# Performance work log

Measured on AMD Instinct MI355X. Metric: run time of the kernel, lower is better.

## Reference

```python
import jax, jax.numpy as jnp
import numpy as np

N_HEAD = 12

def setup_inputs() -> dict:
    key = jax.random.key(0)
    ks = jax.random.split(key, 5)
    B, T, C = 8, 1024, 768
    s = 0.02
    return {
        'x': jax.random.normal(ks[0], (B, T, C), dtype=jnp.float32),
        'w_attn': jax.random.normal(ks[1], (C, 3 * C), dtype=jnp.float32) * s,
        'b_attn': jax.random.normal(ks[2], (3 * C,), dtype=jnp.float32) * s,
        'w_proj': jax.random.normal(ks[3], (C, C), dtype=jnp.float32) * s,
        'b_proj': jax.random.normal(ks[4], (C,), dtype=jnp.float32) * s,
    }

def reference(x, w_attn, b_attn, w_proj, b_proj):
    B, T, C = x.shape
    H, D = N_HEAD, C // N_HEAD
    qkv = x @ w_attn + b_attn                      # [B,T,3C]
    q, k, v = jnp.split(qkv, 3, axis=-1)
    q = q.reshape(B, T, H, D)
    k = k.reshape(B, T, H, D)
    v = v.reshape(B, T, H, D)
    # NOTE: faithful to source - NO 1/sqrt(D) scaling
    wei = jnp.einsum('bthd,bshd->bhts', q, k)      # [B,H,T,T]
    causal = jnp.tril(jnp.ones((T, T), dtype=bool))
    wei = jnp.where(causal[None, None], wei, -jnp.inf)
    wei = jax.nn.softmax(wei, axis=-1)
    out = jnp.einsum('bhts,bshd->bthd', wei, v)    # [B,T,H,D]
    out = out.reshape(B, T, C)
    return out @ w_proj + b_proj
```

## Files before the change

kernel.cpp:

```cpp
#include <hip/hip_runtime.h>

typedef __attribute__((ext_vector_type(8))) short bf16x8_t;
typedef __attribute__((ext_vector_type(4))) float f32x4_t;

#define AS1C(p) ((const __attribute__((address_space(1))) void*)(p))
#define AS3(p)  ((__attribute__((address_space(3))) void*)(p))

#define N_HEAD 12
#define SEQ_T 1024
#define CDIM 768
#define HDIM 64
#define L2E 1.44269504f

__device__ __forceinline__ unsigned short f2bf(float f) {
    union { float f; unsigned int u; } v;
    v.f = f;
    unsigned int r = (v.u + 0x7fffu + ((v.u >> 16) & 1u)) >> 16;
    return (unsigned short)r;
}

__global__ __launch_bounds__(256) void cvt_x(
    const float4* __restrict__ src, ushort4* __restrict__ dst, int n4)
{
    int i = blockIdx.x * 256 + threadIdx.x;
    if (i < n4) {
        float4 v = src[i];
        ushort4 o;
        o.x = f2bf(v.x); o.y = f2bf(v.y); o.z = f2bf(v.z); o.w = f2bf(v.w);
        dst[i] = o;
    }
}

__global__ __launch_bounds__(256) void cvt_transpose(
    const float* __restrict__ src, unsigned short* __restrict__ dst, int R, int Cc)
{
    __shared__ float tile[32][33];
    int c0 = blockIdx.x * 32, r0 = blockIdx.y * 32;
#pragma unroll
    for (int i = 0; i < 4; i++)
        tile[threadIdx.y + i * 8][threadIdx.x] =
            src[(size_t)(r0 + threadIdx.y + i * 8) * Cc + c0 + threadIdx.x];
    __syncthreads();
#pragma unroll
    for (int i = 0; i < 4; i++)
        dst[(size_t)(c0 + threadIdx.y + i * 8) * R + r0 + threadIdx.x] =
            f2bf(tile[threadIdx.x][threadIdx.y + i * 8]);
}

__device__ __forceinline__ void gemm128_core(
    const unsigned short* __restrict__ A, const unsigned short* __restrict__ Bt,
    unsigned short* As, unsigned short* Bs, f32x4_t acc[4][4], int mBase, int nBase)
{
    const int tid  = threadIdx.x;
    const int lane = tid & 63;
    const int wv   = tid >> 6;
    const int quad = lane >> 4;
    const int l16  = lane & 15;
    const int wm   = (wv >> 1) * 64;
    const int wn   = (wv & 1) * 64;

    f32x4_t zero = {0.f, 0.f, 0.f, 0.f};
#pragma unroll
    for (int tm = 0; tm < 4; tm++)
#pragma unroll
        for (int tn = 0; tn < 4; tn++)
            acc[tm][tn] = zero;

    for (int kt = 0; kt < 768; kt += 64) {
#pragma unroll
        for (int i = 0; i < 4; i++) {
            int cbase = i * 256 + wv * 64;
            int ci = cbase + lane;
            int r = ci >> 3;
            int koff = (ci & 7) << 3;
            __builtin_amdgcn_global_load_lds(
                AS1C(A + (size_t)(mBase + r) * 768 + kt + koff),
                AS3(As + cbase * 8), 16, 0, 0);
            __builtin_amdgcn_global_load_lds(
                AS1C(Bt + (size_t)(nBase + r) * 768 + kt + koff),
                AS3(Bs + cbase * 8), 16, 0, 0);
        }
        __syncthreads();
#pragma unroll
        for (int ks = 0; ks < 2; ks++) {
            bf16x8_t af[4], bfv[4];
#pragma unroll
            for (int tm = 0; tm < 4; tm++)
                af[tm] = *(const bf16x8_t*)(As + (wm + tm * 16 + l16) * 64 + ks * 32 + quad * 8);
#pragma unroll
            for (int tn = 0; tn < 4; tn++)
                bfv[tn] = *(const bf16x8_t*)(Bs + (wn + tn * 16 + l16) * 64 + ks * 32 + quad * 8);
#pragma unroll
            for (int tm = 0; tm < 4; tm++)
#pragma unroll
                for (int tn = 0; tn < 4; tn++)
                    acc[tm][tn] = __builtin_amdgcn_mfma_f32_16x16x32_bf16(
                        af[tm], bfv[tn], acc[tm][tn], 0, 0, 0);
        }
        __syncthreads();
    }
}

__global__ __launch_bounds__(256) void gemm_qkv(
    const unsigned short* __restrict__ x, const unsigned short* __restrict__ waT,
    const float* __restrict__ b_attn,
    unsigned short* __restrict__ qbuf, unsigned short* __restrict__ kbuf,
    unsigned short* __restrict__ vbuf)
{
    __shared__ __align__(16) unsigned short As[128 * 64];
    __shared__ __align__(16) unsigned short Bs[128 * 64];
    f32x4_t acc[4][4];
    const int mBase = blockIdx.y * 128;
    const int nBase = blockIdx.x * 128;
    gemm128_core(x, waT, As, Bs, acc, mBase, nBase);

    const int tid = threadIdx.x;
    const int lane = tid & 63, wv = tid >> 6;
    const int quad = lane >> 4, l16 = lane & 15;
    const int wm = (wv >> 1) * 64, wn = (wv & 1) * 64;
    const int part = blockIdx.x / 6;

#pragma unroll
    for (int tn = 0; tn < 4; tn++) {
        int n = nBase + wn + tn * 16 + l16;
        float bv = b_attn[n];
        int f = n - part * 768;
        int hh = f >> 6, d = f & 63;
        if (part == 2) {
#pragma unroll
            for (int tm = 0; tm < 4; tm++) {
                int t0 = mBase + wm + tm * 16 + quad * 4;
                int bb = t0 >> 10, tt = t0 & 1023;
                ushort4 pk;
                pk.x = f2bf(acc[tm][tn][0] + bv);
                pk.y = f2bf(acc[tm][tn][1] + bv);
                pk.z = f2bf(acc[tm][tn][2] + bv);
                pk.w = f2bf(acc[tm][tn][3] + bv);
                *(ushort4*)(vbuf + ((size_t)(bb * N_HEAD + hh) * HDIM + d) * SEQ_T + tt) = pk;
            }
        } else {
            const float scale = (part == 0) ? L2E : 1.f;
            unsigned short* dst = (part == 0) ? qbuf : kbuf;
#pragma unroll
            for (int tm = 0; tm < 4; tm++) {
#pragma unroll
                for (int i = 0; i < 4; i++) {
                    int row = mBase + wm + tm * 16 + quad * 4 + i;
                    int bb = row >> 10, tt = row & 1023;
                    dst[((size_t)(bb * N_HEAD + hh) * SEQ_T + tt) * HDIM + d] =
                        f2bf((acc[tm][tn][i] + bv) * scale);
                }
            }
        }
    }
}

__device__ __forceinline__ void attn_tile(
    const bf16x8_t qf[2], const bf16x8_t kf[4][2], const bf16x8_t vf[4][2],
    f32x4_t o[4], float lsum[4], unsigned short* pw,
    int diag, int wv, int quad, int l16)
{
    f32x4_t zero = {0.f, 0.f, 0.f, 0.f};
    f32x4_t s[4];
#pragma unroll
    for (int c = 0; c < 4; c++) {
        s[c] = zero;
#pragma unroll
        for (int kc = 0; kc < 2; kc++)
            s[c] = __builtin_amdgcn_mfma_f32_16x16x32_bf16(qf[kc], kf[c][kc], s[c], 0, 0, 0);
    }
    if (diag) {
#pragma unroll
        for (int c = 0; c < 4; c++)
#pragma unroll
            for (int i = 0; i < 4; i++)
                if (c * 16 + l16 > wv * 16 + quad * 4 + i) s[c][i] = -1e30f;
    }
    float p[4][4];
#pragma unroll
    for (int c = 0; c < 4; c++)
#pragma unroll
        for (int i = 0; i < 4; i++)
            p[c][i] = exp2f(s[c][i]);
#pragma unroll
    for (int i = 0; i < 4; i++)
        lsum[i] += (p[0][i] + p[1][i]) + (p[2][i] + p[3][i]);

    __asm__ __volatile__("" ::: "memory");
#pragma unroll
    for (int c = 0; c < 4; c++)
#pragma unroll
        for (int i = 0; i < 4; i++) {
            int m = quad * 4 + i;
            pw[m * 64 + (((2 * c + (l16 >> 3)) ^ (m & 7)) << 3) + (l16 & 7)] = f2bf(p[c][i]);
        }
    __asm__ __volatile__("" ::: "memory");
#pragma unroll
    for (int kc = 0; kc < 2; kc++) {
        bf16x8_t pf = *(const bf16x8_t*)(pw + l16 * 64 + (((kc * 4 + quad) ^ (l16 & 7)) << 3));
#pragma unroll
        for (int c = 0; c < 4; c++)
            o[c] = __builtin_amdgcn_mfma_f32_16x16x32_bf16(pf, vf[c][kc], o[c], 0, 0, 0);
    }
}

__global__ __launch_bounds__(256, 3) void attn_fused(
    const unsigned short* __restrict__ qb, const unsigned short* __restrict__ kb,
    const unsigned short* __restrict__ vb, unsigned short* __restrict__ attb)
{
    __shared__ __align__(16) unsigned short Kbuf[2][64 * 64];
    __shared__ __align__(16) unsigned short Vbuf[2][64 * 64];
    __shared__ __align__(16) unsigned short Psh[4][16 * 64];

    const int t = blockIdx.x;
    const int h = blockIdx.y;
    const int b = blockIdx.z;
    const int tid = threadIdx.x;
    const int lane = tid & 63, wv = tid >> 6;
    const int quad = lane >> 4, l16 = lane & 15;
    const int tB = 15 - t, kmax = 15 - t;

    const size_t bh = (size_t)(b * N_HEAD + h);
    const unsigned short* kbase = kb + bh * SEQ_T * HDIM;
    const unsigned short* vbase = vb + bh * HDIM * SEQ_T;
    const unsigned short* qpt   = qb + bh * SEQ_T * HDIM;

    const int j0 = wv * 128 + lane, j1 = j0 + 64;
    const int r0 = j0 >> 3, g0 = (j0 & 7) ^ (r0 & 7);
    const int r1 = j1 >> 3, g1 = (j1 & 7) ^ (r1 & 7);
    const int rgK0 = r0 * 64 + g0 * 8,   rgK1 = r1 * 64 + g1 * 8;
    const int rgV0 = r0 * 1024 + g0 * 8, rgV1 = r1 * 1024 + g1 * 8;
    const int ldsc0 = (wv * 128) * 8, ldsc1 = (wv * 128 + 64) * 8;

    bf16x8_t qfA[2], qfB[2];
    {
        const unsigned short* qa = qpt + (size_t)(t * 64 + wv * 16 + l16) * HDIM;
        const unsigned short* qbp = qpt + (size_t)(tB * 64 + wv * 16 + l16) * HDIM;
#pragma unroll
        for (int kc = 0; kc < 2; kc++) {
            qfA[kc] = *(const bf16x8_t*)(qa + kc * 32 + quad * 8);
            qfB[kc] = *(const bf16x8_t*)(qbp + kc * 32 + quad * 8);
        }
    }

    f32x4_t zero = {0.f, 0.f, 0.f, 0.f};
    f32x4_t oA[4], oB[4];
    float lA[4], lB[4];
#pragma unroll
    for (int c = 0; c < 4; c++) { oA[c] = zero; oB[c] = zero; }
#pragma unroll
    for (int i = 0; i < 4; i++) { lA[i] = 0.f; lB[i] = 0.f; }

    __builtin_amdgcn_global_load_lds(AS1C(kbase + rgK0), AS3(&Kbuf[0][0] + ldsc0), 16, 0, 0);
    __builtin_amdgcn_global_load_lds(AS1C(kbase + rgK1), AS3(&Kbuf[0][0] + ldsc1), 16, 0, 0);
    __builtin_amdgcn_global_load_lds(AS1C(vbase + rgV0), AS3(&Vbuf[0][0] + ldsc0), 16, 0, 0);
    __builtin_amdgcn_global_load_lds(AS1C(vbase + rgV1), AS3(&Vbuf[0][0] + ldsc1), 16, 0, 0);
    __syncthreads();

    for (int kt = 0; kt <= kmax; kt++) {
        const int cur = kt & 1, nxt = cur ^ 1;
        if (kt < kmax) {
            const unsigned short* kp = kbase + (kt + 1) * 4096;
            const unsigned short* vp = vbase + (kt + 1) * 64;
            __builtin_amdgcn_global_load_lds(AS1C(kp + rgK0), AS3(&Kbuf[nxt][0] + ldsc0), 16, 0, 0);
            __builtin_amdgcn_global_load_lds(AS1C(kp + rgK1), AS3(&Kbuf[nxt][0] + ldsc1), 16, 0, 0);
            __builtin_amdgcn_global_load_lds(AS1C(vp + rgV0), AS3(&Vbuf[nxt][0] + ldsc0), 16, 0, 0);
            __builtin_amdgcn_global_load_lds(AS1C(vp + rgV1), AS3(&Vbuf[nxt][0] + ldsc1), 16, 0, 0);
        }

        bf16x8_t kf[4][2], vf[4][2];
        const unsigned short* Kc = &Kbuf[cur][0];
        const unsigned short* Vc = &Vbuf[cur][0];
#pragma unroll
        for (int c = 0; c < 4; c++)
#pragma unroll
            for (int kc = 0; kc < 2; kc++) {
                int roff = (c * 16 + l16) * 64 + (((kc * 4 + quad) ^ (l16 & 7)) << 3);
                kf[c][kc] = *(const bf16x8_t*)(Kc + roff);
                vf[c][kc] = *(const bf16x8_t*)(Vc + roff);
            }

        unsigned short* pw = &Psh[wv][0];
        attn_tile(qfB, kf, vf, oB, lB, pw, kt == tB, wv, quad, l16);
        if (kt <= t)
            attn_tile(qfA, kf, vf, oA, lA, pw, kt == t, wv, quad, l16);
        __syncthreads();
    }

#pragma unroll
    for (int off = 1; off < 16; off <<= 1)
#pragma unroll
        for (int i = 0; i < 4; i++) {
            lA[i] += __shfl_xor(lA[i], off);
            lB[i] += __shfl_xor(lB[i], off);
        }
    float iA[4], iB[4];
#pragma unroll
    for (int i = 0; i < 4; i++) { iA[i] = 1.f / lA[i]; iB[i] = 1.f / lB[i]; }

#pragma unroll
    for (int c = 0; c < 4; c++)
#pragma unroll
        for (int i = 0; i < 4; i++) {
            int rowA = t * 64 + wv * 16 + quad * 4 + i;
            int rowB = tB * 64 + wv * 16 + quad * 4 + i;
            int col = h * HDIM + c * 16 + l16;
            attb[((size_t)b * SEQ_T + rowA) * CDIM + col] = f2bf(oA[c][i] * iA[i]);
            attb[((size_t)b * SEQ_T + rowB) * CDIM + col] = f2bf(oB[c][i] * iB[i]);
        }
}

__global__ __launch_bounds__(256) void gemm_proj(
    const unsigned short* __restrict__ attb, const unsigned short* __restrict__ wpT,
    const float* __restrict__ b_proj, float* __restrict__ out)
{
    __shared__ __align__(16) unsigned short As[128 * 64];
    __shared__ __align__(16) unsigned short Bs[128 * 64];
    f32x4_t acc[4][4];
    const int mBase = blockIdx.y * 128;
    const int nBase = blockIdx.x * 128;
    gemm128_core(attb, wpT, As, Bs, acc, mBase, nBase);

    const int tid = threadIdx.x;
    const int lane = tid & 63, wv = tid >> 6;
    const int quad = lane >> 4, l16 = lane & 15;
    const int wm = (wv >> 1) * 64, wn = (wv & 1) * 64;

#pragma unroll
    for (int tn = 0; tn < 4; tn++) {
        int n = nBase + wn + tn * 16 + l16;
        float bv = b_proj[n];
#pragma unroll
        for (int tm = 0; tm < 4; tm++)
#pragma unroll
            for (int i = 0; i < 4; i++) {
                int row = mBase + wm + tm * 16 + quad * 4 + i;
                out[(size_t)row * CDIM + n] = acc[tm][tn][i] + bv;
            }
    }
}

extern "C" void kernel_launch(void* const* d_in, const int* in_sizes, int n_in,
                              void* d_out, int out_size, void* d_ws, size_t ws_size,
                              hipStream_t stream) {
    const float* x      = (const float*)d_in[0];
    const float* w_attn = (const float*)d_in[1];
    const float* b_attn = (const float*)d_in[2];
    const float* w_proj = (const float*)d_in[3];
    const float* b_proj = (const float*)d_in[4];
    float* out = (float*)d_out;

    unsigned short* ws   = (unsigned short*)d_ws;
    unsigned short* waT  = ws;
    unsigned short* wpT  = waT + 1769472;
    unsigned short* xbf  = wpT + 589824;
    unsigned short* qbuf = xbf + 6291456;
    unsigned short* kbuf = qbuf + 6291456;
    unsigned short* vbuf = kbuf + 6291456;
    unsigned short* attb = vbuf + 6291456;

    cvt_x<<<dim3(6144), 256, 0, stream>>>((const float4*)x, (ushort4*)xbf, 1572864);
    cvt_transpose<<<dim3(72, 24), dim3(32, 8), 0, stream>>>(w_attn, waT, 768, 2304);
    cvt_transpose<<<dim3(24, 24), dim3(32, 8), 0, stream>>>(w_proj, wpT, 768, 768);
    gemm_qkv<<<dim3(18, 64), 256, 0, stream>>>(xbf, waT, b_attn, qbuf, kbuf, vbuf);
    attn_fused<<<dim3(8, N_HEAD, 8), 256, 0, stream>>>(qbuf, kbuf, vbuf, attb);
    gemm_proj<<<dim3(6, 64), 256, 0, stream>>>(attb, wpT, b_proj, out);
}
```

Baseline: 212.1 us.

## Swizzle GEMM LDS tiles and transpose attention score MFMA for packed P writes

The shared GEMM core now XOR-swizzles the 16-byte chunk index on both the global-to-LDS load and the fragment read, to cut LDS bank conflicts. The attention kernel computes S^T (K as the A operand, Q as B), so each lane holds one query row. The row sum therefore needs only two cross-lane shuffles, and P can be written to LDS as packed 32-bit pairs instead of scalar 16-bit stores. K fragments are now loaded per column block and shared between the two query tiles, with the extra cost of per-row inverse shuffles in the epilogue.

```diff
diff --git a/kernel.cpp b/kernel.cpp
--- a/kernel.cpp
+++ b/kernel.cpp
@@ -72,7 +72,7 @@
             int cbase = i * 256 + wv * 64;
             int ci = cbase + lane;
             int r = ci >> 3;
-            int koff = (ci & 7) << 3;
+            int koff = (((ci & 7) ^ (r & 7)) << 3);
             __builtin_amdgcn_global_load_lds(
                 AS1C(A + (size_t)(mBase + r) * 768 + kt + koff),
                 AS3(As + cbase * 8), 16, 0, 0);
@@ -86,10 +86,12 @@
             bf16x8_t af[4], bfv[4];
 #pragma unroll
             for (int tm = 0; tm < 4; tm++)
-                af[tm] = *(const bf16x8_t*)(As + (wm + tm * 16 + l16) * 64 + ks * 32 + quad * 8);
+                af[tm] = *(const bf16x8_t*)(As + (wm + tm * 16 + l16) * 64 +
+                                            (((ks * 4 + quad) ^ (l16 & 7)) << 3));
 #pragma unroll
             for (int tn = 0; tn < 4; tn++)
-                bfv[tn] = *(const bf16x8_t*)(Bs + (wn + tn * 16 + l16) * 64 + ks * 32 + quad * 8);
+                bfv[tn] = *(const bf16x8_t*)(Bs + (wn + tn * 16 + l16) * 64 +
+                                             (((ks * 4 + quad) ^ (l16 & 7)) << 3));
 #pragma unroll
             for (int tm = 0; tm < 4; tm++)
 #pragma unroll
@@ -155,26 +157,16 @@
     }
 }
 
-__device__ __forceinline__ void attn_tile(
-    const bf16x8_t qf[2], const bf16x8_t kf[4][2], const bf16x8_t vf[4][2],
-    f32x4_t o[4], float lsum[4], unsigned short* pw,
-    int diag, int wv, int quad, int l16)
-{
-    f32x4_t zero = {0.f, 0.f, 0.f, 0.f};
-    f32x4_t s[4];
-#pragma unroll
-    for (int c = 0; c < 4; c++) {
-        s[c] = zero;
-#pragma unroll
-        for (int kc = 0; kc < 2; kc++)
-            s[c] = __builtin_amdgcn_mfma_f32_16x16x32_bf16(qf[kc], kf[c][kc], s[c], 0, 0, 0);
-    }
+__device__ __forceinline__ void attn_pv(
+    f32x4_t s[4], int diag, int qloc, int quad, int l16,
+    float& lsum, unsigned short* pw, const bf16x8_t vf[4][2], f32x4_t o[4])
+{
     if (diag) {
 #pragma unroll
         for (int c = 0; c < 4; c++)
 #pragma unroll
             for (int i = 0; i < 4; i++)
-                if (c * 16 + l16 > wv * 16 + quad * 4 + i) s[c][i] = -1e30f;
+                if (c * 16 + quad * 4 + i > qloc) s[c][i] = -1e30f;
     }
     float p[4][4];
 #pragma unroll
@@ -183,25 +175,37 @@
         for (int i = 0; i < 4; i++)
             p[c][i] = exp2f(s[c][i]);
 #pragma unroll
-    for (int i = 0; i < 4; i++)
-        lsum[i] += (p[0][i] + p[1][i]) + (p[2][i] + p[3][i]);
+    for (int c = 0; c < 4; c++)
+        lsum += (p[c][0] + p[c][1]) + (p[c][2] + p[c][3]);
+
+    unsigned int u[4][2];
+#pragma unroll
+    for (int c = 0; c < 4; c++)
+#pragma unroll
+        for (int i2 = 0; i2 < 2; i2++)
+            u[c][i2] = (unsigned int)f2bf(p[c][2 * i2]) |
+                       ((unsigned int)f2bf(p[c][2 * i2 + 1]) << 16);
 
     __asm__ __volatile__("" ::: "memory");
 #pragma unroll
     for (int c = 0; c < 4; c++)
 #pragma unroll
-        for (int i = 0; i < 4; i++) {
-            int m = quad * 4 + i;
-            pw[m * 64 + (((2 * c + (l16 >> 3)) ^ (m & 7)) << 3) + (l16 & 7)] = f2bf(p[c][i]);
+        for (int i2 = 0; i2 < 2; i2++) {
+            int g = c * 2 + (quad >> 1);
+            *(unsigned int*)(pw + l16 * 64 + ((g ^ (l16 & 7)) << 3) +
+                             4 * (quad & 1) + 2 * i2) = u[c][i2];
         }
     __asm__ __volatile__("" ::: "memory");
-#pragma unroll
-    for (int kc = 0; kc < 2; kc++) {
-        bf16x8_t pf = *(const bf16x8_t*)(pw + l16 * 64 + (((kc * 4 + quad) ^ (l16 & 7)) << 3));
-#pragma unroll
-        for (int c = 0; c < 4; c++)
-            o[c] = __builtin_amdgcn_mfma_f32_16x16x32_bf16(pf, vf[c][kc], o[c], 0, 0, 0);
-    }
+    bf16x8_t pf[2];
+#pragma unroll
+    for (int kc = 0; kc < 2; kc++)
+        pf[kc] = *(const bf16x8_t*)(pw + l16 * 64 + (((kc * 4 + quad) ^ (l16 & 7)) << 3));
+    __asm__ __volatile__("" ::: "memory");
+#pragma unroll
+    for (int kc = 0; kc < 2; kc++)
+#pragma unroll
+        for (int nc = 0; nc < 4; nc++)
+            o[nc] = __builtin_amdgcn_mfma_f32_16x16x32_bf16(pf[kc], vf[nc][kc], o[nc], 0, 0, 0);
 }
 
 __global__ __launch_bounds__(256, 3) void attn_fused(
@@ -219,6 +223,7 @@
     const int lane = tid & 63, wv = tid >> 6;
     const int quad = lane >> 4, l16 = lane & 15;
     const int tB = 15 - t, kmax = 15 - t;
+    const int qloc = wv * 16 + l16;
 
     const size_t bh = (size_t)(b * N_HEAD + h);
     const unsigned short* kbase = kb + bh * SEQ_T * HDIM;
@@ -234,8 +239,8 @@
 
     bf16x8_t qfA[2], qfB[2];
     {
-        const unsigned short* qa = qpt + (size_t)(t * 64 + wv * 16 + l16) * HDIM;
-        const unsigned short* qbp = qpt + (size_t)(tB * 64 + wv * 16 + l16) * HDIM;
+        const unsigned short* qa  = qpt + (size_t)(t * 64 + qloc) * HDIM;
+        const unsigned short* qbp = qpt + (size_t)(tB * 64 + qloc) * HDIM;
 #pragma unroll
         for (int kc = 0; kc < 2; kc++) {
             qfA[kc] = *(const bf16x8_t*)(qa + kc * 32 + quad * 8);
@@ -245,11 +250,9 @@
 
     f32x4_t zero = {0.f, 0.f, 0.f, 0.f};
     f32x4_t oA[4], oB[4];
-    float lA[4], lB[4];
 #pragma unroll
     for (int c = 0; c < 4; c++) { oA[c] = zero; oB[c] = zero; }
-#pragma unroll
-    for (int i = 0; i < 4; i++) { lA[i] = 0.f; lB[i] = 0.f; }
+    float lA = 0.f, lB = 0.f;
 
     __builtin_amdgcn_global_load_lds(AS1C(kbase + rgK0), AS3(&Kbuf[0][0] + ldsc0), 16, 0, 0);
     __builtin_amdgcn_global_load_lds(AS1C(kbase + rgK1), AS3(&Kbuf[0][0] + ldsc1), 16, 0, 0);
@@ -268,45 +271,59 @@
             __builtin_amdgcn_global_load_lds(AS1C(vp + rgV1), AS3(&Vbuf[nxt][0] + ldsc1), 16, 0, 0);
         }
 
-        bf16x8_t kf[4][2], vf[4][2];
         const unsigned short* Kc = &Kbuf[cur][0];
         const unsigned short* Vc = &Vbuf[cur][0];
-#pragma unroll
-        for (int c = 0; c < 4; c++)
-#pragma unroll
-            for (int kc = 0; kc < 2; kc++) {
-                int roff = (c * 16 + l16) * 64 + (((kc * 4 + quad) ^ (l16 & 7)) << 3);
-                kf[c][kc] = *(const bf16x8_t*)(Kc + roff);
-                vf[c][kc] = *(const bf16x8_t*)(Vc + roff);
+        const int doA = (kt <= t);
+
+        bf16x8_t vf[4][2];
+#pragma unroll
+        for (int nc = 0; nc < 4; nc++)
+#pragma unroll
+            for (int kc = 0; kc < 2; kc++)
+                vf[nc][kc] = *(const bf16x8_t*)(Vc + (nc * 16 + l16) * 64 +
+                                                (((kc * 4 + quad) ^ (l16 & 7)) << 3));
+
+        f32x4_t sB[4], sA[4];
+#pragma unroll
+        for (int c = 0; c < 4; c++) {
+            bf16x8_t kf0 = *(const bf16x8_t*)(Kc + (c * 16 + l16) * 64 +
+                                              ((quad ^ (l16 & 7)) << 3));
+            bf16x8_t kf1 = *(const bf16x8_t*)(Kc + (c * 16 + l16) * 64 +
+                                              (((4 + quad) ^ (l16 & 7)) << 3));
+            sB[c] = __builtin_amdgcn_mfma_f32_16x16x32_bf16(kf0, qfB[0], zero, 0, 0, 0);
+            sB[c] = __builtin_amdgcn_mfma_f32_16x16x32_bf16(kf1, qfB[1], sB[c], 0, 0, 0);
+            if (doA) {
+                sA[c] = __builtin_amdgcn_mfma_f32_16x16x32_bf16(kf0, qfA[0], zero, 0, 0, 0);
+                sA[c] = __builtin_amdgcn_mfma_f32_16x16x32_bf16(kf1, qfA[1], sA[c], 0, 0, 0);
             }
+        }
 
         unsigned short* pw = &Psh[wv][0];
-        attn_tile(qfB, kf, vf, oB, lB, pw, kt == tB, wv, quad, l16);
-        if (kt <= t)
-            attn_tile(qfA, kf, vf, oA, lA, pw, kt == t, wv, quad, l16);
+        attn_pv(sB, kt == tB, qloc, quad, l16, lB, pw, vf, oB);
+        if (doA)
+            attn_pv(sA, kt == t, qloc, quad, l16, lA, pw, vf, oA);
         __syncthreads();
     }
 
-#pragma unroll
-    for (int off = 1; off < 16; off <<= 1)
-#pragma unroll
-        for (int i = 0; i < 4; i++) {
-            lA[i] += __shfl_xor(lA[i], off);
-            lB[i] += __shfl_xor(lB[i], off);
-        }
+    lA += __shfl_xor(lA, 16); lA += __shfl_xor(lA, 32);
+    lB += __shfl_xor(lB, 16); lB += __shfl_xor(lB, 32);
+    float invA = 1.f / lA, invB = 1.f / lB;
     float iA[4], iB[4];
 #pragma unroll
-    for (int i = 0; i < 4; i++) { iA[i] = 1.f / lA[i]; iB[i] = 1.f / lB[i]; }
-
-#pragma unroll
-    for (int c = 0; c < 4; c++)
+    for (int i = 0; i < 4; i++) {
+        iA[i] = __shfl(invA, quad * 4 + i);
+        iB[i] = __shfl(invB, quad * 4 + i);
+    }
+
+#pragma unroll
+    for (int nc = 0; nc < 4; nc++)
 #pragma unroll
         for (int i = 0; i < 4; i++) {
             int rowA = t * 64 + wv * 16 + quad * 4 + i;
             int rowB = tB * 64 + wv * 16 + quad * 4 + i;
-            int col = h * HDIM + c * 16 + l16;
-            attb[((size_t)b * SEQ_T + rowA) * CDIM + col] = f2bf(oA[c][i] * iA[i]);
-            attb[((size_t)b * SEQ_T + rowB) * CDIM + col] = f2bf(oB[c][i] * iB[i]);
+            int col = h * HDIM + nc * 16 + l16;
+            attb[((size_t)b * SEQ_T + rowA) * CDIM + col] = f2bf(oA[nc][i] * iA[i]);
+            attb[((size_t)b * SEQ_T + rowB) * CDIM + col] = f2bf(oB[nc][i] * iB[i]);
         }
 }
 
```

Result: faster. 199.4 us (-6.0%).
